# Kernel optimization log

Measured on AMD Instinct MI355X. Metric: run time of the kernel, lower is better.

## Reference

```python
import jax, jax.numpy as jnp
import numpy as np

IN_CH, OUT_CH, MODES = 64, 64, 16
BATCH, N = 64, 8192


def setup_inputs() -> dict:
    key = jax.random.key(0)
    k1, k2, k3 = jax.random.split(key, 3)
    scale = 1.0 / (IN_CH * OUT_CH)
    x = jax.random.normal(k1, (BATCH, IN_CH, N), dtype=jnp.float32)
    w_real = scale * jax.random.uniform(k2, (IN_CH, OUT_CH, MODES), dtype=jnp.float32)
    w_imag = scale * jax.random.uniform(k3, (IN_CH, OUT_CH, MODES), dtype=jnp.float32)
    return {"x": x, "w_real": w_real, "w_imag": w_imag}


def reference(x, w_real, w_imag):
    # x: (b, in_ch, n) real. weights: (in_ch, out_ch, modes) complex.
    n = x.shape[-1]
    weights = w_real + 1j * w_imag                      # complex64
    x_ft = jnp.fft.rfft(x)                              # (b, in_ch, n//2+1) complex
    # multiply only the lowest `modes` frequencies by learned complex weights
    out_modes = jnp.einsum('bix,iox->box', x_ft[:, :, :MODES], weights)
    n_freq = n // 2 + 1
    out_ft = jnp.zeros((x.shape[0], OUT_CH, n_freq), dtype=jnp.complex64)
    out_ft = out_ft.at[:, :, :MODES].set(out_modes)
    return jnp.fft.irfft(out_ft, n=n)                   # (b, out_ch, n) real
```

## Files before the change

kernel.cpp:

```cpp
#include <hip/hip_runtime.h>

#define NPTS 8192

typedef __bf16 bf16x8 __attribute__((ext_vector_type(8)));
typedef short short8 __attribute__((ext_vector_type(8)));
typedef float f32x4 __attribute__((ext_vector_type(4)));


__global__ __launch_bounds__(256) void prep_kernel(const float* __restrict__ wr,
                                                   const float* __restrict__ wi,
                                                   float* __restrict__ wtr,
                                                   float* __restrict__ wti,
                                                   ushort* __restrict__ bas) {
    const int bid = blockIdx.x, t = threadIdx.x;
    if (bid < 256) {
        int idx = bid * 256 + t;
        int i = idx >> 10, o = (idx >> 4) & 63, k = idx & 15;
        int dst = k * 4096 + i * 64 + o;
        wtr[dst] = wr[idx];
        wti[dst] = wi[idx];
    } else {
        int e = (bid - 256) * 256 + t;
        int j = e & 7;
        int lane = (e >> 3) & 63;
        int gk = (e >> 9) & 255;
        int ct = e >> 17;
        int m = lane & 15;
        int n = gk * 32 + ((lane >> 4) & 3) * 8 + j;
        int p = (m * n) & 8191;
        float a = (float)p * (1.0f / 4096.0f);
        float v = ct ? -sinpif(a) : cospif(a);
        unsigned u = __float_as_uint(v);
        unsigned hb = (u + 0x7fffu + ((u >> 16) & 1u)) >> 16;
        float hf = __uint_as_float(hb << 16);
        float lo = v - hf;
        unsigned ul = __float_as_uint(lo);
        unsigned lb = (ul + 0x7fffu + ((ul >> 16) & 1u)) >> 16;
        bas[e] = (ushort)hb;
        bas[262144 + e] = (ushort)lb;
    }
}

__global__ __launch_bounds__(256) void dft_kernel(const float* __restrict__ x,
                                                  const ushort* __restrict__ bas,
                                                  float* __restrict__ Xp) {
    const int t = threadIdx.x;
    const int lane = t & 63, w = t >> 6;
    const int rb = blockIdx.x >> 4, seg = blockIdx.x & 15;
    const int rowq = lane >> 4;
    const int row = rb * 64 + w * 16 + (lane & 15);
    const float* xp = x + (size_t)row * NPTS + seg * 512 + rowq * 8;
    const bf16x8* bh = (const bf16x8*)bas;
    const bf16x8* bl = (const bf16x8*)(bas + 262144);
    const int gk0 = seg * 16;

    f32x4 acc0 = {0.f, 0.f, 0.f, 0.f};
    f32x4 acc1 = {0.f, 0.f, 0.f, 0.f};

    float4 xa = *(const float4*)xp;
    float4 xb = *(const float4*)(xp + 4);
    bf16x8 c0h = bh[gk0 * 64 + lane];
    bf16x8 c1h = bh[(256 + gk0) * 64 + lane];
    bf16x8 c0l = bl[gk0 * 64 + lane];
    bf16x8 c1l = bl[(256 + gk0) * 64 + lane];

    for (int ks = 0; ks < 16; ++ks) {
        short8 hsv, lsv;
        {
            float v[8] = {xa.x, xa.y, xa.z, xa.w, xb.x, xb.y, xb.z, xb.w};
#pragma unroll
            for (int j = 0; j < 8; ++j) {
                unsigned u = __float_as_uint(v[j]);
                hsv[j] = (short)(u >> 16);
                float lo = v[j] - __uint_as_float(u & 0xffff0000u);
                unsigned ul = __float_as_uint(lo);
                lsv[j] = (short)((ul + 0x7fffu + ((ul >> 16) & 1u)) >> 16);
            }
        }
        bf16x8 ah = __builtin_bit_cast(bf16x8, hsv);
        bf16x8 al = __builtin_bit_cast(bf16x8, lsv);

        float4 nxa, nxb;
        bf16x8 n0h, n1h, n0l, n1l;
        if (ks < 15) {
            const float* xq = xp + (ks + 1) * 32;
            nxa = *(const float4*)xq;
            nxb = *(const float4*)(xq + 4);
            int gk = gk0 + ks + 1;
            n0h = bh[gk * 64 + lane];
            n1h = bh[(256 + gk) * 64 + lane];
            n0l = bl[gk * 64 + lane];
            n1l = bl[(256 + gk) * 64 + lane];
        }

        acc0 = __builtin_amdgcn_mfma_f32_16x16x32_bf16(ah, c0h, acc0, 0, 0, 0);
        acc1 = __builtin_amdgcn_mfma_f32_16x16x32_bf16(ah, c1h, acc1, 0, 0, 0);
        acc0 = __builtin_amdgcn_mfma_f32_16x16x32_bf16(al, c0h, acc0, 0, 0, 0);
        acc1 = __builtin_amdgcn_mfma_f32_16x16x32_bf16(al, c1h, acc1, 0, 0, 0);
        acc0 = __builtin_amdgcn_mfma_f32_16x16x32_bf16(ah, c0l, acc0, 0, 0, 0);
        acc1 = __builtin_amdgcn_mfma_f32_16x16x32_bf16(ah, c1l, acc1, 0, 0, 0);

        if (ks < 15) {
            xa = nxa; xb = nxb;
            c0h = n0h; c1h = n1h; c0l = n0l; c1l = n1l;
        }
    }

    const int k = lane & 15;
    const int rbase = rb * 64 + w * 16 + rowq * 4;
    *(f32x4*)&Xp[(size_t)((seg * 16 + k) * 2 + 0) * 4096 + rbase] = acc0;
    *(f32x4*)&Xp[(size_t)((seg * 16 + k) * 2 + 1) * 4096 + rbase] = acc1;
}

__global__ __launch_bounds__(256) void mix_kernel(const float* __restrict__ Xp,
                                                  const float* __restrict__ wtr,
                                                  const float* __restrict__ wti,
                                                  float* __restrict__ yc) {
    __shared__ float xre[16 * 65], xim[16 * 65];
    __shared__ float wlr[4096], wli[4096];
    const int t = threadIdx.x;
    const int k = blockIdx.x & 15, bq = blockIdx.x >> 4;
#pragma unroll
    for (int j = 0; j < 4; ++j) {
        int lr = t + j * 256;
        int row = bq * 1024 + lr;
        float re = 0.f, im = 0.f;
#pragma unroll
        for (int s = 0; s < 16; ++s) {
            re += Xp[((s * 16 + k) * 2 + 0) * 4096 + row];
            im += Xp[((s * 16 + k) * 2 + 1) * 4096 + row];
        }
        xre[(lr >> 6) * 65 + (lr & 63)] = re;
        xim[(lr >> 6) * 65 + (lr & 63)] = im;
        ((float4*)wlr)[t + j * 256] = ((const float4*)(wtr + k * 4096))[t + j * 256];
        ((float4*)wli)[t + j * 256] = ((const float4*)(wti + k * 4096))[t + j * 256];
    }
    __syncthreads();
    const int bt = t >> 4;
    const int o4 = t & 15;
    float accr[4] = {0.f, 0.f, 0.f, 0.f}, acci[4] = {0.f, 0.f, 0.f, 0.f};
    for (int i = 0; i < 64; ++i) {
        float xr = xre[bt * 65 + i], xi = xim[bt * 65 + i];
        float4 w4r = ((const float4*)wlr)[i * 16 + o4];
        float4 w4i = ((const float4*)wli)[i * 16 + o4];
        accr[0] += xr * w4r.x - xi * w4i.x;  acci[0] += xr * w4i.x + xi * w4r.x;
        accr[1] += xr * w4r.y - xi * w4i.y;  acci[1] += xr * w4i.y + xi * w4r.y;
        accr[2] += xr * w4r.z - xi * w4i.z;  acci[2] += xr * w4i.z + xi * w4r.z;
        accr[3] += xr * w4r.w - xi * w4i.w;  acci[3] += xr * w4i.w + xi * w4r.w;
    }
    const float invn = 1.0f / 8192.0f;
#pragma unroll
    for (int oo = 0; oo < 4; ++oo) {
        int row = (bq * 16 + bt) * 64 + o4 * 4 + oo;
        if (k == 0) {
            yc[row * 32]      = accr[oo] * invn;
            yc[row * 32 + 16] = 0.f;
        } else {
            yc[row * 32 + k]      = 2.f * accr[oo] * invn;
            yc[row * 32 + 16 + k] = -2.f * acci[oo] * invn;
        }
    }
}

__global__ __launch_bounds__(256) void synth_kernel(const float* __restrict__ yc,
                                                    float* __restrict__ out) {
    __shared__ float cf[512];
    const int t = threadIdx.x;
    const int rg = blockIdx.x >> 4, tile = blockIdx.x & 15;
    cf[t]       = yc[rg * 512 + t];
    cf[t + 256] = yc[rg * 512 + 256 + t];

    const int n0 = tile * 512 + t * 2;
    float2 cb[16], sb[16];
    cb[0] = make_float2(1.f, 1.f);
    sb[0] = make_float2(0.f, 0.f);
    {
        float a0 = (float)(n0 & 8191) * (1.0f / 4096.0f);
        float a1 = (float)((n0 + 1) & 8191) * (1.0f / 4096.0f);
        cb[1] = make_float2(cospif(a0), cospif(a1));
        sb[1] = make_float2(sinpif(a0), sinpif(a1));
    }
#pragma unroll
    for (int k = 2; k < 16; ++k) {
        cb[k] = make_float2(cb[k-1].x * cb[1].x - sb[k-1].x * sb[1].x,
                            cb[k-1].y * cb[1].y - sb[k-1].y * sb[1].y);
        sb[k] = make_float2(sb[k-1].x * cb[1].x + cb[k-1].x * sb[1].x,
                            sb[k-1].y * cb[1].y + cb[k-1].y * sb[1].y);
    }
    __syncthreads();
#pragma unroll 4
    for (int r = 0; r < 16; ++r) {
        const float4* c4 = (const float4*)&cf[r * 32];
        float ax = 0.f, ay = 0.f;
#pragma unroll
        for (int j = 0; j < 4; ++j) {
            float4 a = c4[j];
            float4 s = c4[4 + j];
            ax += a.x * cb[4*j].x + a.y * cb[4*j+1].x + a.z * cb[4*j+2].x + a.w * cb[4*j+3].x
                + s.x * sb[4*j].x + s.y * sb[4*j+1].x + s.z * sb[4*j+2].x + s.w * sb[4*j+3].x;
            ay += a.x * cb[4*j].y + a.y * cb[4*j+1].y + a.z * cb[4*j+2].y + a.w * cb[4*j+3].y
                + s.x * sb[4*j].y + s.y * sb[4*j+1].y + s.z * sb[4*j+2].y + s.w * sb[4*j+3].y;
        }
        *(float2*)&out[(rg * 16 + r) * NPTS + n0] = make_float2(ax, ay);
    }
}

extern "C" void kernel_launch(void* const* d_in, const int* in_sizes, int n_in,
                              void* d_out, int out_size, void* d_ws, size_t ws_size,
                              hipStream_t stream) {
    const float* x  = (const float*)d_in[0];
    const float* wr = (const float*)d_in[1];
    const float* wi = (const float*)d_in[2];
    float* out = (float*)d_out;
    float* ws  = (float*)d_ws;
    float* yc  = ws;
    float* wtr = ws + 131072;
    float* wti = ws + 196608;
    float* Xp  = out;
    ushort* bas = (ushort*)(out + 2097152);

    prep_kernel<<<1280, 256, 0, stream>>>(wr, wi, wtr, wti, bas);
    dft_kernel<<<1024, 256, 0, stream>>>(x, bas, Xp);
    mix_kernel<<<64, 256, 0, stream>>>(Xp, wtr, wti, yc);
    synth_kernel<<<4096, 256, 0, stream>>>(yc, out);
}
```

Measured before the change: 282.3 us.

## Move inverse DFT synthesis onto bf16x3 MFMA and spread mix over more blocks

The synthesis stage is rewritten to use 16x16x32 bf16 MFMAs with a hi/lo split (three MFMAs per tile), replacing the scalar FMA dot products over 32 coefficients. The twiddle basis for each lane is advanced by incremental complex rotation across 32 iterations. Mix now launches four times as many blocks, each computing one output per thread. This cuts VALU work in the dominant write-bound synth stage, but the rotation recurrence and the bf16x3 split can add rounding error.

```diff
diff --git a/kernel.cpp b/kernel.cpp
--- a/kernel.cpp
+++ b/kernel.cpp
@@ -6,6 +6,17 @@
 typedef short short8 __attribute__((ext_vector_type(8)));
 typedef float f32x4 __attribute__((ext_vector_type(4)));
 
+
+__device__ __forceinline__ void split8(const float* v, short8& h, short8& l) {
+#pragma unroll
+    for (int j = 0; j < 8; ++j) {
+        unsigned u = __float_as_uint(v[j]);
+        h[j] = (short)(u >> 16);
+        float lo = v[j] - __uint_as_float(u & 0xffff0000u);
+        unsigned ul = __float_as_uint(lo);
+        l[j] = (short)((ul + 0x7fffu + ((ul >> 16) & 1u)) >> 16);
+    }
+}
 
 __global__ __launch_bounds__(256) void prep_kernel(const float* __restrict__ wr,
                                                    const float* __restrict__ wi,
@@ -65,18 +76,9 @@
     bf16x8 c1l = bl[(256 + gk0) * 64 + lane];
 
     for (int ks = 0; ks < 16; ++ks) {
+        float v[8] = {xa.x, xa.y, xa.z, xa.w, xb.x, xb.y, xb.z, xb.w};
         short8 hsv, lsv;
-        {
-            float v[8] = {xa.x, xa.y, xa.z, xa.w, xb.x, xb.y, xb.z, xb.w};
-#pragma unroll
-            for (int j = 0; j < 8; ++j) {
-                unsigned u = __float_as_uint(v[j]);
-                hsv[j] = (short)(u >> 16);
-                float lo = v[j] - __uint_as_float(u & 0xffff0000u);
-                unsigned ul = __float_as_uint(lo);
-                lsv[j] = (short)((ul + 0x7fffu + ((ul >> 16) & 1u)) >> 16);
-            }
-        }
+        split8(v, hsv, lsv);
         bf16x8 ah = __builtin_bit_cast(bf16x8, hsv);
         bf16x8 al = __builtin_bit_cast(bf16x8, lsv);
 
@@ -116,92 +118,107 @@
                                                   const float* __restrict__ wtr,
                                                   const float* __restrict__ wti,
                                                   float* __restrict__ yc) {
-    __shared__ float xre[16 * 65], xim[16 * 65];
+    __shared__ float xre[256], xim[256];
     __shared__ float wlr[4096], wli[4096];
     const int t = threadIdx.x;
     const int k = blockIdx.x & 15, bq = blockIdx.x >> 4;
-#pragma unroll
-    for (int j = 0; j < 4; ++j) {
-        int lr = t + j * 256;
-        int row = bq * 1024 + lr;
+    {
+        int row = bq * 256 + t;
         float re = 0.f, im = 0.f;
 #pragma unroll
         for (int s = 0; s < 16; ++s) {
             re += Xp[((s * 16 + k) * 2 + 0) * 4096 + row];
             im += Xp[((s * 16 + k) * 2 + 1) * 4096 + row];
         }
-        xre[(lr >> 6) * 65 + (lr & 63)] = re;
-        xim[(lr >> 6) * 65 + (lr & 63)] = im;
-        ((float4*)wlr)[t + j * 256] = ((const float4*)(wtr + k * 4096))[t + j * 256];
-        ((float4*)wli)[t + j * 256] = ((const float4*)(wti + k * 4096))[t + j * 256];
+        xre[t] = re;
+        xim[t] = im;
+#pragma unroll
+        for (int j = 0; j < 4; ++j) {
+            ((float4*)wlr)[t + j * 256] = ((const float4*)(wtr + k * 4096))[t + j * 256];
+            ((float4*)wli)[t + j * 256] = ((const float4*)(wti + k * 4096))[t + j * 256];
+        }
     }
     __syncthreads();
-    const int bt = t >> 4;
-    const int o4 = t & 15;
-    float accr[4] = {0.f, 0.f, 0.f, 0.f}, acci[4] = {0.f, 0.f, 0.f, 0.f};
+    const int bt = t >> 6;
+    const int o = t & 63;
+    float accr = 0.f, acci = 0.f;
+#pragma unroll 8
     for (int i = 0; i < 64; ++i) {
-        float xr = xre[bt * 65 + i], xi = xim[bt * 65 + i];
-        float4 w4r = ((const float4*)wlr)[i * 16 + o4];
-        float4 w4i = ((const float4*)wli)[i * 16 + o4];
-        accr[0] += xr * w4r.x - xi * w4i.x;  acci[0] += xr * w4i.x + xi * w4r.x;
-        accr[1] += xr * w4r.y - xi * w4i.y;  acci[1] += xr * w4i.y + xi * w4r.y;
-        accr[2] += xr * w4r.z - xi * w4i.z;  acci[2] += xr * w4i.z + xi * w4r.z;
-        accr[3] += xr * w4r.w - xi * w4i.w;  acci[3] += xr * w4i.w + xi * w4r.w;
+        float xr = xre[bt * 64 + i], xi = xim[bt * 64 + i];
+        float wr = wlr[i * 64 + o], wi = wli[i * 64 + o];
+        accr += xr * wr - xi * wi;
+        acci += xr * wi + xi * wr;
     }
     const float invn = 1.0f / 8192.0f;
-#pragma unroll
-    for (int oo = 0; oo < 4; ++oo) {
-        int row = (bq * 16 + bt) * 64 + o4 * 4 + oo;
-        if (k == 0) {
-            yc[row * 32]      = accr[oo] * invn;
-            yc[row * 32 + 16] = 0.f;
-        } else {
-            yc[row * 32 + k]      = 2.f * accr[oo] * invn;
-            yc[row * 32 + 16 + k] = -2.f * acci[oo] * invn;
-        }
+    int row2 = (bq * 4 + bt) * 64 + o;
+    if (k == 0) {
+        yc[row2 * 32]      = accr * invn;
+        yc[row2 * 32 + 16] = 0.f;
+    } else {
+        yc[row2 * 32 + k]      = 2.f * accr * invn;
+        yc[row2 * 32 + 16 + k] = -2.f * acci * invn;
     }
 }
 
 __global__ __launch_bounds__(256) void synth_kernel(const float* __restrict__ yc,
                                                     float* __restrict__ out) {
-    __shared__ float cf[512];
     const int t = threadIdx.x;
-    const int rg = blockIdx.x >> 4, tile = blockIdx.x & 15;
-    cf[t]       = yc[rg * 512 + t];
-    cf[t + 256] = yc[rg * 512 + 256 + t];
-
-    const int n0 = tile * 512 + t * 2;
-    float2 cb[16], sb[16];
-    cb[0] = make_float2(1.f, 1.f);
-    sb[0] = make_float2(0.f, 0.f);
+    const int lane = t & 63, w = t >> 6;
+    const int rg = blockIdx.x >> 2, nq = blockIdx.x & 3;
+    const int rowbase = rg * 16;
+    const int col = lane & 15;
+    const int q = lane >> 4;
+    const int fb = (q & 1) * 8;
+    const bool isSin = q >= 2;
+
+    bf16x8 bhf, blf;
     {
-        float a0 = (float)(n0 & 8191) * (1.0f / 4096.0f);
-        float a1 = (float)((n0 + 1) & 8191) * (1.0f / 4096.0f);
-        cb[1] = make_float2(cospif(a0), cospif(a1));
-        sb[1] = make_float2(sinpif(a0), sinpif(a1));
-    }
-#pragma unroll
-    for (int k = 2; k < 16; ++k) {
-        cb[k] = make_float2(cb[k-1].x * cb[1].x - sb[k-1].x * sb[1].x,
-                            cb[k-1].y * cb[1].y - sb[k-1].y * sb[1].y);
-        sb[k] = make_float2(sb[k-1].x * cb[1].x + cb[k-1].x * sb[1].x,
-                            sb[k-1].y * cb[1].y + cb[k-1].y * sb[1].y);
-    }
-    __syncthreads();
+        float v[8];
+        const float* cp = yc + (rowbase + col) * 32 + q * 8;
+        *(float4*)&v[0] = *(const float4*)cp;
+        *(float4*)&v[4] = *(const float4*)(cp + 4);
+        short8 h, l;
+        split8(v, h, l);
+        bhf = __builtin_bit_cast(bf16x8, h);
+        blf = __builtin_bit_cast(bf16x8, l);
+    }
+
+    float val[8], aux[8], cd[8], sd[8];
+    const int nbase = nq * 2048 + w * 512;
+    {
+        int n = nbase + col;
+#pragma unroll
+        for (int j = 0; j < 8; ++j) {
+            int fj = fb + j;
+            float a = (float)((fj * n) & 8191) * (1.0f / 4096.0f);
+            float c = cospif(a), s = sinpif(a);
+            val[j] = isSin ? s : c;
+            aux[j] = isSin ? -c : s;
+            float b = (float)fj * (1.0f / 256.0f);
+            cd[j] = cospif(b);
+            sd[j] = sinpif(b);
+        }
+    }
+
+    float* op = out + (size_t)(rowbase + col) * NPTS + nbase + q * 4;
 #pragma unroll 4
-    for (int r = 0; r < 16; ++r) {
-        const float4* c4 = (const float4*)&cf[r * 32];
-        float ax = 0.f, ay = 0.f;
-#pragma unroll
-        for (int j = 0; j < 4; ++j) {
-            float4 a = c4[j];
-            float4 s = c4[4 + j];
-            ax += a.x * cb[4*j].x + a.y * cb[4*j+1].x + a.z * cb[4*j+2].x + a.w * cb[4*j+3].x
-                + s.x * sb[4*j].x + s.y * sb[4*j+1].x + s.z * sb[4*j+2].x + s.w * sb[4*j+3].x;
-            ay += a.x * cb[4*j].y + a.y * cb[4*j+1].y + a.z * cb[4*j+2].y + a.w * cb[4*j+3].y
-                + s.x * sb[4*j].y + s.y * sb[4*j+1].y + s.z * sb[4*j+2].y + s.w * sb[4*j+3].y;
-        }
-        *(float2*)&out[(rg * 16 + r) * NPTS + n0] = make_float2(ax, ay);
+    for (int it = 0; it < 32; ++it) {
+        short8 h, l;
+        split8(val, h, l);
+        bf16x8 ah = __builtin_bit_cast(bf16x8, h);
+        bf16x8 al = __builtin_bit_cast(bf16x8, l);
+        f32x4 acc = {0.f, 0.f, 0.f, 0.f};
+        acc = __builtin_amdgcn_mfma_f32_16x16x32_bf16(ah, bhf, acc, 0, 0, 0);
+        acc = __builtin_amdgcn_mfma_f32_16x16x32_bf16(al, bhf, acc, 0, 0, 0);
+        acc = __builtin_amdgcn_mfma_f32_16x16x32_bf16(ah, blf, acc, 0, 0, 0);
+        *(f32x4*)(op + it * 16) = acc;
+#pragma unroll
+        for (int j = 0; j < 8; ++j) {
+            float nv = val[j] * cd[j] - aux[j] * sd[j];
+            float na = aux[j] * cd[j] + val[j] * sd[j];
+            val[j] = nv;
+            aux[j] = na;
+        }
     }
 }
 
@@ -221,6 +238,6 @@
 
     prep_kernel<<<1280, 256, 0, stream>>>(wr, wi, wtr, wti, bas);
     dft_kernel<<<1024, 256, 0, stream>>>(x, bas, Xp);
-    mix_kernel<<<64, 256, 0, stream>>>(Xp, wtr, wti, yc);
-    synth_kernel<<<4096, 256, 0, stream>>>(yc, out);
-}
+    mix_kernel<<<256, 256, 0, stream>>>(Xp, wtr, wti, yc);
+    synth_kernel<<<1024, 256, 0, stream>>>(yc, out);
+}
```

Result: faster. 258.3 us (-8.5%).
